# Kernel optimization log

Measured on AMD Instinct MI355X. Metric: run time of the kernel, lower is better.

## Reference

```python
import jax, jax.numpy as jnp
import numpy as np

N = 50000      # n_nodes
S = 16         # neighbors per node
D_IN = 256     # raw feature dim
PREP = 128     # prep_len
H = 2          # n_head
OUT = 64       # per-head spec output_dim (concat_node doubles it)
MP = 2         # n_mp (metapaths)
IN2 = 2 * OUT * H  # layer-2 input dim = 256


def setup_inputs() -> dict:
    key = jax.random.key(0)
    ks = jax.random.split(key, 7)
    feats = jax.random.normal(ks[0], (N, D_IN), jnp.float32)
    prep_W = jax.random.normal(ks[1], (D_IN, PREP), jnp.float32) * 0.05
    Wx1 = jax.random.normal(ks[2], (MP, H, PREP, OUT), jnp.float32) * 0.05
    Wn1 = jax.random.normal(ks[3], (MP, H, PREP, OUT), jnp.float32) * 0.05
    Wx2 = jax.random.normal(ks[4], (MP, H, IN2, OUT), jnp.float32) * 0.05
    Wn2 = jax.random.normal(ks[5], (MP, H, IN2, OUT), jnp.float32) * 0.05
    node_neigh = jax.random.randint(ks[6], (MP, N, S), 0, N, dtype=jnp.int32)
    return {"feats": feats, "prep_W": prep_W, "Wx1": Wx1, "Wn1": Wn1,
            "Wx2": Wx2, "Wn2": Wn2, "node_neigh": node_neigh}


def _agg_layer(x, neigh, Wx, Wn):
    # x: [N, d]; neigh: [N, S]; Wx, Wn: [H, d, OUT]
    # neighbor gather + mean (the chunk_edge = all_feats[node_neigh] path)
    agg = jnp.mean(x[neigh], axis=1)                  # [N, d]
    xh = jnp.einsum('nd,hdo->nho', x, Wx)             # [N, H, OUT]
    nh = jnp.einsum('nd,hdo->nho', agg, Wn)           # [N, H, OUT]
    h = jax.nn.relu(jnp.concatenate([xh, nh], -1))    # per-head concat_node
    return h.reshape(x.shape[0], -1)                  # heads concatenated


def reference(feats, prep_W, Wx1, Wn1, Wx2, Wn2, node_neigh):
    # feats[all_ids].detach() in the original -> stop_gradient
    feats = jax.lax.stop_gradient(feats)
    outs = []
    for mp in range(MP):
        h0 = feats @ prep_W                           # prep (dummy == layer-1 prep here)
        neigh = node_neigh[mp]
        h1 = _agg_layer(h0, neigh, Wx1[mp], Wn1[mp])  # [N, 256]
        h2 = _agg_layer(h1, neigh, Wx2[mp], Wn2[mp])  # [N, 256]
        outs.append(jnp.concatenate([h1, h2], axis=-1))  # skip-buffer concat
    return jnp.stack(outs, axis=0)                    # [MP, N, 512]
```

## Files before the change

### kernel.cpp

```cpp
#include <hip/hip_runtime.h>

#define NN 50000
#define SNEI 16
#define GB 782

typedef unsigned short ushort_t;
typedef unsigned int uint_t;
typedef unsigned long long u64;
typedef __attribute__((ext_vector_type(8))) short bhalf8;
typedef __attribute__((ext_vector_type(4))) float facc4;
typedef __attribute__((ext_vector_type(4))) float f32x4;
typedef __attribute__((ext_vector_type(4))) int i32x4;
typedef __attribute__((ext_vector_type(4))) uint_t u32x4;

__device__ __forceinline__ float b2f(uint_t u) {
    union { uint_t u; float f; } x; x.u = u << 16; return x.f;
}
__device__ __forceinline__ ushort_t f2b(float f) {
    union { float f; uint_t u; } x; x.f = f;
    return (ushort_t)((x.u + 0x7FFFu + ((x.u >> 16) & 1u)) >> 16);
}
__device__ __forceinline__ u64 pack4(float a, float b, float c, float d) {
    return (u64)f2b(a) | ((u64)f2b(b) << 16) | ((u64)f2b(c) << 32) | ((u64)f2b(d) << 48);
}

typedef const __attribute__((address_space(1))) void cglb_t;
typedef __attribute__((address_space(3))) void lds3_t;
__device__ __forceinline__ void gload16(const void* g, void* l) {
    __builtin_amdgcn_global_load_lds((cglb_t*)g, (lds3_t*)l, 16, 0, 0);
}

__global__ void permSetup(const float* __restrict__ prepW,
                          const float* __restrict__ Wx1, const float* __restrict__ Wn1,
                          const float* __restrict__ Wx2, const float* __restrict__ Wn2,
                          ushort_t* __restrict__ dst)
{
    int e = blockIdx.x * 256 + threadIdx.x;
    int q8 = e >> 3, j = e & 7;
    int layer = q8 >> 14;
    int qq = q8 & 16383;
    int mp = qq >> 13, isN = (qq >> 12) & 1, q = qq & 4095;
    int lane = q & 63, nf = (q >> 6) & 7, ks = q >> 9;
    int c = nf * 16 + (lane & 15);
    int k = ks * 32 + ((lane >> 4) << 3) + j;
    float v;
    if (layer == 0) {
        const float* W1 = (isN ? Wn1 : Wx1) + mp * 16384 + (c >> 6) * 8192 + (c & 63);
        const float* pw = prepW + (size_t)k * 128;
        float s0 = 0.f, s1 = 0.f;
#pragma unroll 4
        for (int p = 0; p < 128; p += 2) {
            s0 += pw[p]     * W1[(size_t)p * 64];
            s1 += pw[p + 1] * W1[(size_t)(p + 1) * 64];
        }
        v = s0 + s1;
    } else {
        const float* W2 = (isN ? Wn2 : Wx2) + mp * 32768 + (c >> 6) * 16384 + (size_t)k * 64 + (c & 63);
        v = *W2;
    }
    dst[(size_t)q8 * 8 + j] = f2b(v);
}

__global__ __launch_bounds__(512, 4)
void proj1_gemm(const float* __restrict__ X,
                const ushort_t* __restrict__ W, size_t wMpStr,
                float* __restrict__ out, size_t oMpStr,
                ushort_t* __restrict__ h1, size_t hMpStr,
                ushort_t* __restrict__ P, size_t PMpStr)
{
    __shared__ bhalf8 lds[4608];
    u64* l64 = (u64*)lds;
    const int tid = threadIdx.x;
    const int lane = tid & 63;
    const int wid = tid >> 6;
    const int wave_m = wid >> 2;
    const int role = wid & 3;
    const int mp = role >> 1, isN = role & 1;
    const int m0 = blockIdx.x * 64;

    facc4 acc[2][8];
    const facc4 z = {0.f, 0.f, 0.f, 0.f};
#pragma unroll
    for (int i = 0; i < 2; ++i)
#pragma unroll
        for (int j = 0; j < 8; ++j) acc[i][j] = z;

    for (int kt = 0; kt < 4; ++kt) {
        {
            int s = tid;
            int fp = s >> 6, ls = s & 63;
            int mf = fp & 3, ksl = fp >> 2;
            int row = m0 + mf * 16 + (ls & 15); if (row > NN - 1) row = NN - 1;
            const f32x4* gp = (const f32x4*)(X + (size_t)row * 256 + kt * 64 + ksl * 32 + ((ls >> 4) << 3));
            f32x4 f0 = gp[0], f1 = gp[1];
            l64[s * 2]     = pack4(f0[0], f0[1], f0[2], f0[3]);
            l64[s * 2 + 1] = pack4(f1[0], f1[1], f1[2], f1[3]);
        }
#pragma unroll
        for (int it = 0; it < 8; ++it) {
            int c4 = it * 512 + tid;
            int m = c4 >> 10, c = c4 & 1023;
            const ushort_t* src = W + (size_t)(m >> 1) * wMpStr + (m & 1) * 32768
                                + ((size_t)kt * 1024 + c) * 8;
            gload16(src, (char*)lds + (512 + m * 1024 + c) * 16);
        }
        __syncthreads();
        const int wB = 512 + role * 1024;
#pragma unroll
        for (int ksl = 0; ksl < 2; ++ksl) {
            bhalf8 a0 = lds[(ksl * 4 + wave_m * 2 + 0) * 64 + lane];
            bhalf8 a1 = lds[(ksl * 4 + wave_m * 2 + 1) * 64 + lane];
#pragma unroll
            for (int nf = 0; nf < 8; ++nf) {
                bhalf8 b = lds[wB + (ksl * 8 + nf) * 64 + lane];
                acc[0][nf] = __builtin_amdgcn_mfma_f32_16x16x32_bf16(a0, b, acc[0][nf], 0, 0, 0);
                acc[1][nf] = __builtin_amdgcn_mfma_f32_16x16x32_bf16(a1, b, acc[1][nf], 0, 0, 0);
            }
        }
        __syncthreads();
    }
    const int cl = lane & 15, rg = lane >> 4;
    if (isN == 0) {
        float* xl = (float*)lds + mp * (64 * 132);
#pragma unroll
        for (int mf2 = 0; mf2 < 2; ++mf2) {
            int rowl = (wave_m * 2 + mf2) * 16 + rg * 4;
#pragma unroll
            for (int nf = 0; nf < 8; ++nf) {
                int cpr = nf * 16 + cl;
                facc4 v = acc[mf2][nf];
#pragma unroll
                for (int rr = 0; rr < 4; ++rr)
                    xl[(rowl + rr) * 132 + cpr] = fmaxf(v[rr], 0.0f);
            }
        }
    } else {
        ushort_t* Pp = P + (size_t)mp * PMpStr;
#pragma unroll
        for (int mf2 = 0; mf2 < 2; ++mf2) {
            int rowb = m0 + (wave_m * 2 + mf2) * 16 + rg * 4;
#pragma unroll
            for (int nf = 0; nf < 8; ++nf) {
                int cpr = nf * 16 + cl;
                facc4 v = acc[mf2][nf];
#pragma unroll
                for (int rr = 0; rr < 4; ++rr) {
                    int row = rowb + rr;
                    if (row < NN)
                        Pp[(size_t)(cpr >> 5) * (NN * 32) + (size_t)row * 32 + (cpr & 31)] = f2b(v[rr]);
                }
            }
        }
    }
    __syncthreads();
#pragma unroll
    for (int it = 0; it < 8; ++it) {
        int u = it * 512 + tid;
        int seg = u >> 4, l16 = u & 15;
        int mp2 = seg >> 7, rowl = (seg >> 1) & 63, ch = seg & 1;
        int row = m0 + rowl;
        f32x4 v = *(f32x4*)((float*)lds + mp2 * (64 * 132) + rowl * 132 + ch * 64 + l16 * 4);
        if (row < NN) {
            __builtin_nontemporal_store(v,
                (f32x4*)(out + (size_t)mp2 * oMpStr + (size_t)row * 512 + ch * 128 + l16 * 4));
            *(u64*)(h1 + (size_t)mp2 * hMpStr + (size_t)row * 256 + ch * 128 + l16 * 4)
                = pack4(v[0], v[1], v[2], v[3]);
        }
    }
}

__global__ __launch_bounds__(256, 4)
void proj2_gemm(const ushort_t* __restrict__ X, size_t xMpStr,
                const ushort_t* __restrict__ W, size_t wMpStr,
                float* __restrict__ out, size_t oMpStr,
                ushort_t* __restrict__ P, size_t PMpStr)
{
    __shared__ bhalf8 lds[2560];
    const int tid = threadIdx.x;
    const int lane = tid & 63;
    const int wid = tid >> 6;
    const int wave_m = wid >> 1, wave_n = wid & 1;
    const int m0 = blockIdx.x * 64;
    const int mp = blockIdx.y;

    const ushort_t* Xp = X + (size_t)mp * xMpStr;
    const ushort_t* wx = W + (size_t)mp * wMpStr;
    const ushort_t* wn = wx + 4096 * 8;
    float* outp = out + (size_t)mp * oMpStr;
    ushort_t* Pp = P + (size_t)mp * PMpStr;

    facc4 acc[2][8];
    const facc4 z = {0.f, 0.f, 0.f, 0.f};
#pragma unroll
    for (int i = 0; i < 2; ++i)
#pragma unroll
        for (int j = 0; j < 8; ++j) acc[i][j] = z;

    for (int kt = 0; kt < 4; ++kt) {
#pragma unroll
        for (int it = 0; it < 2; ++it) {
            int u = wid + it * 4;
            int mf = u & 3, ksl = u >> 2;
            int row = m0 + mf * 16 + (lane & 15); if (row > NN - 1) row = NN - 1;
            const ushort_t* src = Xp + (size_t)row * 256 + kt * 64 + ksl * 32 + ((lane >> 4) << 3);
            gload16(src, (char*)lds + (u * 64 + lane) * 16);
        }
#pragma unroll
        for (int it = 0; it < 4; ++it) {
            int cb = (it * 4 + wid) * 64;
            gload16(wx + ((size_t)kt * 1024 + cb + lane) * 8,
                    (char*)lds + (512 + cb + lane) * 16);
            gload16(wn + ((size_t)kt * 1024 + cb + lane) * 8,
                    (char*)lds + (1536 + cb + lane) * 16);
        }
        __syncthreads();
        const int wB = wave_n ? 1536 : 512;
#pragma unroll
        for (int ksl = 0; ksl < 2; ++ksl) {
            bhalf8 a0 = lds[(ksl * 4 + wave_m * 2 + 0) * 64 + lane];
            bhalf8 a1 = lds[(ksl * 4 + wave_m * 2 + 1) * 64 + lane];
#pragma unroll
            for (int nf = 0; nf < 8; ++nf) {
                bhalf8 b = lds[wB + (ksl * 8 + nf) * 64 + lane];
                acc[0][nf] = __builtin_amdgcn_mfma_f32_16x16x32_bf16(a0, b, acc[0][nf], 0, 0, 0);
                acc[1][nf] = __builtin_amdgcn_mfma_f32_16x16x32_bf16(a1, b, acc[1][nf], 0, 0, 0);
            }
        }
        __syncthreads();
    }
    const int cl = lane & 15, rg = lane >> 4;
    float* xl = (float*)lds;
    if (wave_n == 0) {
#pragma unroll
        for (int mf2 = 0; mf2 < 2; ++mf2) {
            int rowl = (wave_m * 2 + mf2) * 16 + rg * 4;
#pragma unroll
            for (int nf = 0; nf < 8; ++nf) {
                int cpr = nf * 16 + cl;
                facc4 v = acc[mf2][nf];
#pragma unroll
                for (int rr = 0; rr < 4; ++rr)
                    xl[(rowl + rr) * 132 + cpr] = fmaxf(v[rr], 0.0f);
            }
        }
    } else {
#pragma unroll
        for (int mf2 = 0; mf2 < 2; ++mf2) {
            int rowb = m0 + (wave_m * 2 + mf2) * 16 + rg * 4;
#pragma unroll
            for (int nf = 0; nf < 8; ++nf) {
                int cpr = nf * 16 + cl;
                facc4 v = acc[mf2][nf];
#pragma unroll
                for (int rr = 0; rr < 4; ++rr) {
                    int row = rowb + rr;
                    if (row < NN)
                        Pp[(size_t)(cpr >> 5) * (NN * 32) + (size_t)row * 32 + (cpr & 31)] = f2b(v[rr]);
                }
            }
        }
    }
    __syncthreads();
#pragma unroll
    for (int j = 0; j < 4; ++j) {
        int rowl2 = wid * 16 + j * 4 + (lane >> 4);
        int row = m0 + rowl2;
#pragma unroll
        for (int c = 0; c < 2; ++c) {
            f32x4 v = *(f32x4*)&xl[rowl2 * 132 + c * 64 + cl * 4];
            if (row < NN)
                __builtin_nontemporal_store(v,
                    (f32x4*)&outp[(size_t)row * 512 + 256 + c * 128 + cl * 4]);
        }
    }
}

template<bool WRH1>
__global__ __launch_bounds__(256)
void gatherS(const ushort_t* __restrict__ P, size_t PMpStr,
             const int* __restrict__ nb, size_t nMpStr,
             float* __restrict__ out, size_t oMpStr, int obase,
             ushort_t* __restrict__ h1, size_t hMpStr)
{
    const int b = blockIdx.x;
    const int pair = b & 7;
    const int slice = pair & 3, mp = pair >> 2;
    const int nodeBase = (b >> 3) * 64;

    const ushort_t* Pp = P + (size_t)mp * PMpStr + (size_t)slice * (NN * 32);
    const int* nbp = nb + (size_t)mp * nMpStr;
    float* outp = out + (size_t)mp * oMpStr;

    __shared__ int nls[1024];
    __shared__ float og[64 * 36];
    {
        int i4 = nodeBase * 4 + threadIdx.x;
        int mx = NN * 4 - 1;
        if (i4 > mx) i4 = mx;
        i32x4 v = __builtin_nontemporal_load((const i32x4*)nbp + i4);
        ((i32x4*)nls)[threadIdx.x] = v;
    }
    __syncthreads();

    const int nl = threadIdx.x >> 2, q = threadIdx.x & 3;
    const int node = nodeBase + nl;
    const int* nr = nls + nl * SNEI;
    float a0=0.f,a1=0.f,a2=0.f,a3=0.f,a4=0.f,a5=0.f,a6=0.f,a7=0.f;
#pragma unroll
    for (int s = 0; s < SNEI; ++s) {
        u32x4 v = *(const u32x4*)(Pp + (size_t)nr[s] * 32 + q * 8);
        a0 += b2f(v.x & 0xFFFFu); a1 += b2f(v.x >> 16);
        a2 += b2f(v.y & 0xFFFFu); a3 += b2f(v.y >> 16);
        a4 += b2f(v.z & 0xFFFFu); a5 += b2f(v.z >> 16);
        a6 += b2f(v.w & 0xFFFFu); a7 += b2f(v.w >> 16);
    }
    const float M = 0.0625f;
    f32x4 r0 = { fmaxf(a0*M, 0.f), fmaxf(a1*M, 0.f), fmaxf(a2*M, 0.f), fmaxf(a3*M, 0.f) };
    f32x4 r1 = { fmaxf(a4*M, 0.f), fmaxf(a5*M, 0.f), fmaxf(a6*M, 0.f), fmaxf(a7*M, 0.f) };
    const int cco = (slice >> 1) * 128 + 64 + (slice & 1) * 32 + q * 8;
    if constexpr (WRH1) {
        if (node < NN) {
            ushort_t* hp = h1 + (size_t)mp * hMpStr + (size_t)node * 256 + cco;
            *(u64*)hp       = pack4(r0[0], r0[1], r0[2], r0[3]);
            *(u64*)(hp + 4) = pack4(r1[0], r1[1], r1[2], r1[3]);
        }
    }
    *(f32x4*)&og[nl * 36 + q * 8]     = r0;
    *(f32x4*)&og[nl * 36 + q * 8 + 4] = r1;
    __syncthreads();

    const int coff0 = (slice >> 1) * 128 + 64 + (slice & 1) * 32;
#pragma unroll
    for (int it = 0; it < 2; ++it) {
        int rl = it * 32 + (threadIdx.x >> 3), sub = threadIdx.x & 7;
        int nd = nodeBase + rl;
        f32x4 v = *(f32x4*)&og[rl * 36 + sub * 4];
        if (nd < NN)
            __builtin_nontemporal_store(v,
                (f32x4*)(outp + (size_t)nd * 512 + obase + coff0 + sub * 4));
    }
}

extern "C" void kernel_launch(void* const* d_in, const int* in_sizes, int n_in,
                              void* d_out, int out_size, void* d_ws, size_t ws_size,
                              hipStream_t stream)
{
    const float* feats  = (const float*)d_in[0];
    const float* prepWp = (const float*)d_in[1];
    const float* Wx1    = (const float*)d_in[2];
    const float* Wn1    = (const float*)d_in[3];
    const float* Wx2    = (const float*)d_in[4];
    const float* Wn2    = (const float*)d_in[5];
    const int*   neigh  = (const int*)d_in[6];
    float* out = (float*)d_out;
    ushort_t* ws = (ushort_t*)d_ws;

    const size_t permElems = 262144;
    ushort_t* perm = ws;
    ushort_t* P    = ws + permElems;
    ushort_t* h1   = P + 2 * (size_t)NN * 128;

    const size_t PStr = (size_t)NN * 128;
    const size_t hStr = (size_t)NN * 256;
    const size_t oStr = (size_t)NN * 512;
    const size_t nStr = (size_t)NN * SNEI;
    const size_t wStr = (size_t)8192 * 8;

    permSetup<<<1024, 256, 0, stream>>>(prepWp, Wx1, Wn1, Wx2, Wn2, perm);

    proj1_gemm<<<GB, 512, 0, stream>>>(feats, perm, wStr,
                                       out, oStr, h1, hStr, P, PStr);
    gatherS<true><<<GB * 8, 256, 0, stream>>>(P, PStr, neigh, nStr,
                                              out, oStr, 0, h1, hStr);
    proj2_gemm<<<dim3(GB, 2), 256, 0, stream>>>(h1, hStr,
                                                perm + (size_t)16384 * 8, wStr,
                                                out, oStr, P, PStr);
    gatherS<false><<<GB * 8, 256, 0, stream>>>(P, PStr, neigh, nStr,
                                               out, oStr, 256, nullptr, 0);
}
```

Before: 173.7 us.

## Fuse layer-1 neighbor gather into layer-2 projection kernel

```diff
diff --git a/kernel.cpp b/kernel.cpp
--- a/kernel.cpp
+++ b/kernel.cpp
@@ -65,8 +65,8 @@
 void proj1_gemm(const float* __restrict__ X,
                 const ushort_t* __restrict__ W, size_t wMpStr,
                 float* __restrict__ out, size_t oMpStr,
-                ushort_t* __restrict__ h1, size_t hMpStr,
-                ushort_t* __restrict__ P, size_t PMpStr)
+                ushort_t* __restrict__ h1x, size_t hMpStr,
+                ushort_t* __restrict__ P1, size_t PMpStr)
 {
     __shared__ bhalf8 lds[4608];
     u64* l64 = (u64*)lds;
@@ -135,7 +135,7 @@
             }
         }
     } else {
-        ushort_t* Pp = P + (size_t)mp * PMpStr;
+        ushort_t* Pp = P1 + (size_t)mp * PMpStr;
 #pragma unroll
         for (int mf2 = 0; mf2 < 2; ++mf2) {
             int rowb = m0 + (wave_m * 2 + mf2) * 16 + rg * 4;
@@ -147,7 +147,7 @@
                 for (int rr = 0; rr < 4; ++rr) {
                     int row = rowb + rr;
                     if (row < NN)
-                        Pp[(size_t)(cpr >> 5) * (NN * 32) + (size_t)row * 32 + (cpr & 31)] = f2b(v[rr]);
+                        Pp[(size_t)row * 128 + cpr] = f2b(v[rr]);
                 }
             }
         }
@@ -163,17 +163,19 @@
         if (row < NN) {
             __builtin_nontemporal_store(v,
                 (f32x4*)(out + (size_t)mp2 * oMpStr + (size_t)row * 512 + ch * 128 + l16 * 4));
-            *(u64*)(h1 + (size_t)mp2 * hMpStr + (size_t)row * 256 + ch * 128 + l16 * 4)
+            *(u64*)(h1x + (size_t)mp2 * hMpStr + (size_t)row * 128 + ch * 64 + l16 * 4)
                 = pack4(v[0], v[1], v[2], v[3]);
         }
     }
 }
 
 __global__ __launch_bounds__(256, 4)
-void proj2_gemm(const ushort_t* __restrict__ X, size_t xMpStr,
-                const ushort_t* __restrict__ W, size_t wMpStr,
-                float* __restrict__ out, size_t oMpStr,
-                ushort_t* __restrict__ P, size_t PMpStr)
+void proj2f(const ushort_t* __restrict__ h1x, size_t hMpStr,
+            const ushort_t* __restrict__ P1, size_t P1MpStr,
+            const int* __restrict__ nb, size_t nMpStr,
+            const ushort_t* __restrict__ W, size_t wMpStr,
+            float* __restrict__ out, size_t oMpStr,
+            ushort_t* __restrict__ P2, size_t P2MpStr)
 {
     __shared__ bhalf8 lds[2560];
     const int tid = threadIdx.x;
@@ -183,11 +185,57 @@
     const int m0 = blockIdx.x * 64;
     const int mp = blockIdx.y;
 
-    const ushort_t* Xp = X + (size_t)mp * xMpStr;
+    const ushort_t* hx = h1x + (size_t)mp * hMpStr;
+    const ushort_t* Pp1 = P1 + (size_t)mp * P1MpStr;
+    const int* nbp = nb + (size_t)mp * nMpStr;
     const ushort_t* wx = W + (size_t)mp * wMpStr;
     const ushort_t* wn = wx + 4096 * 8;
     float* outp = out + (size_t)mp * oMpStr;
-    ushort_t* Pp = P + (size_t)mp * PMpStr;
+    ushort_t* Pp2 = P2 + (size_t)mp * P2MpStr;
+
+    int* nls = (int*)lds;
+    {
+        int i4 = m0 * 4 + tid;
+        int mx = NN * 4 - 1;
+        if (i4 > mx) i4 = mx;
+        ((i32x4*)nls)[tid] = __builtin_nontemporal_load((const i32x4*)nbp + i4);
+    }
+    __syncthreads();
+
+    const int nl = tid >> 2, q = tid & 3;
+    const int node = m0 + nl;
+    const int* nr = nls + nl * SNEI;
+    float ac[32];
+#pragma unroll
+    for (int i = 0; i < 32; ++i) ac[i] = 0.f;
+#pragma unroll 4
+    for (int s = 0; s < SNEI; ++s) {
+        const ushort_t* src = Pp1 + (size_t)nr[s] * 128 + q * 32;
+#pragma unroll
+        for (int g = 0; g < 4; ++g) {
+            u32x4 v = *(const u32x4*)(src + g * 8);
+            ac[g*8+0] += b2f(v.x & 0xFFFFu); ac[g*8+1] += b2f(v.x >> 16);
+            ac[g*8+2] += b2f(v.y & 0xFFFFu); ac[g*8+3] += b2f(v.y >> 16);
+            ac[g*8+4] += b2f(v.z & 0xFFFFu); ac[g*8+5] += b2f(v.z >> 16);
+            ac[g*8+6] += b2f(v.w & 0xFFFFu); ac[g*8+7] += b2f(v.w >> 16);
+        }
+    }
+    const float M = 0.0625f;
+#pragma unroll
+    for (int i = 0; i < 32; ++i) ac[i] = fmaxf(ac[i] * M, 0.f);
+    if (node < NN) {
+        float* o = outp + (size_t)node * 512 + (q >> 1) * 128 + 64 + (q & 1) * 32;
+#pragma unroll
+        for (int g = 0; g < 8; ++g) {
+            f32x4 v = { ac[g*4], ac[g*4+1], ac[g*4+2], ac[g*4+3] };
+            __builtin_nontemporal_store(v, (f32x4*)(o + g * 4));
+        }
+    }
+    u64 st[8];
+#pragma unroll
+    for (int g = 0; g < 8; ++g)
+        st[g] = pack4(ac[g*4], ac[g*4+1], ac[g*4+2], ac[g*4+3]);
+    __syncthreads();
 
     facc4 acc[2][8];
     const facc4 z = {0.f, 0.f, 0.f, 0.f};
@@ -197,13 +245,25 @@
         for (int j = 0; j < 8; ++j) acc[i][j] = z;
 
     for (int kt = 0; kt < 4; ++kt) {
-#pragma unroll
-        for (int it = 0; it < 2; ++it) {
-            int u = wid + it * 4;
-            int mf = u & 3, ksl = u >> 2;
-            int row = m0 + mf * 16 + (lane & 15); if (row > NN - 1) row = NN - 1;
-            const ushort_t* src = Xp + (size_t)row * 256 + kt * 64 + ksl * 32 + ((lane >> 4) << 3);
-            gload16(src, (char*)lds + (u * 64 + lane) * 16);
+        if ((kt & 1) == 0) {
+#pragma unroll
+            for (int it = 0; it < 2; ++it) {
+                int u = wid + it * 4;
+                int mf = u & 3, ksl = u >> 2;
+                int row = m0 + mf * 16 + (lane & 15); if (row > NN - 1) row = NN - 1;
+                const ushort_t* src = hx + (size_t)row * 128 + (kt >> 1) * 64 + ksl * 32 + ((lane >> 4) << 3);
+                gload16(src, (char*)lds + (u * 64 + lane) * 16);
+            }
+        } else {
+            if ((q >> 1) == (kt >> 1)) {
+                int ksl = q & 1, r = nl;
+#pragma unroll
+                for (int g = 0; g < 4; ++g) {
+                    int chunk = (ksl * 4 + (r >> 4)) * 64 + g * 16 + (r & 15);
+                    u64* d = (u64*)&lds[chunk];
+                    d[0] = st[g * 2]; d[1] = st[g * 2 + 1];
+                }
+            }
         }
 #pragma unroll
         for (int it = 0; it < 4; ++it) {
@@ -255,7 +315,7 @@
                 for (int rr = 0; rr < 4; ++rr) {
                     int row = rowb + rr;
                     if (row < NN)
-                        Pp[(size_t)(cpr >> 5) * (NN * 32) + (size_t)row * 32 + (cpr & 31)] = f2b(v[rr]);
+                        Pp2[(size_t)(cpr >> 5) * (NN * 32) + (size_t)row * 32 + (cpr & 31)] = f2b(v[rr]);
                 }
             }
         }
@@ -275,12 +335,10 @@
     }
 }
 
-template<bool WRH1>
 __global__ __launch_bounds__(256)
 void gatherS(const ushort_t* __restrict__ P, size_t PMpStr,
              const int* __restrict__ nb, size_t nMpStr,
-             float* __restrict__ out, size_t oMpStr, int obase,
-             ushort_t* __restrict__ h1, size_t hMpStr)
+             float* __restrict__ out, size_t oMpStr)
 {
     const int b = blockIdx.x;
     const int pair = b & 7;
@@ -297,13 +355,11 @@
         int i4 = nodeBase * 4 + threadIdx.x;
         int mx = NN * 4 - 1;
         if (i4 > mx) i4 = mx;
-        i32x4 v = __builtin_nontemporal_load((const i32x4*)nbp + i4);
-        ((i32x4*)nls)[threadIdx.x] = v;
+        ((i32x4*)nls)[threadIdx.x] = __builtin_nontemporal_load((const i32x4*)nbp + i4);
     }
     __syncthreads();
 
     const int nl = threadIdx.x >> 2, q = threadIdx.x & 3;
-    const int node = nodeBase + nl;
     const int* nr = nls + nl * SNEI;
     float a0=0.f,a1=0.f,a2=0.f,a3=0.f,a4=0.f,a5=0.f,a6=0.f,a7=0.f;
 #pragma unroll
@@ -317,14 +373,6 @@
     const float M = 0.0625f;
     f32x4 r0 = { fmaxf(a0*M, 0.f), fmaxf(a1*M, 0.f), fmaxf(a2*M, 0.f), fmaxf(a3*M, 0.f) };
     f32x4 r1 = { fmaxf(a4*M, 0.f), fmaxf(a5*M, 0.f), fmaxf(a6*M, 0.f), fmaxf(a7*M, 0.f) };
-    const int cco = (slice >> 1) * 128 + 64 + (slice & 1) * 32 + q * 8;
-    if constexpr (WRH1) {
-        if (node < NN) {
-            ushort_t* hp = h1 + (size_t)mp * hMpStr + (size_t)node * 256 + cco;
-            *(u64*)hp       = pack4(r0[0], r0[1], r0[2], r0[3]);
-            *(u64*)(hp + 4) = pack4(r1[0], r1[1], r1[2], r1[3]);
-        }
-    }
     *(f32x4*)&og[nl * 36 + q * 8]     = r0;
     *(f32x4*)&og[nl * 36 + q * 8 + 4] = r1;
     __syncthreads();
@@ -337,7 +385,7 @@
         f32x4 v = *(f32x4*)&og[rl * 36 + sub * 4];
         if (nd < NN)
             __builtin_nontemporal_store(v,
-                (f32x4*)(outp + (size_t)nd * 512 + obase + coff0 + sub * 4));
+                (f32x4*)(outp + (size_t)nd * 512 + 256 + coff0 + sub * 4));
     }
 }
 
@@ -356,12 +404,12 @@
     ushort_t* ws = (ushort_t*)d_ws;
 
     const size_t permElems = 262144;
+    const size_t NP = (size_t)NN * 128;
     ushort_t* perm = ws;
-    ushort_t* P    = ws + permElems;
-    ushort_t* h1   = P + 2 * (size_t)NN * 128;
-
-    const size_t PStr = (size_t)NN * 128;
-    const size_t hStr = (size_t)NN * 256;
+    ushort_t* P1   = ws + permElems;
+    ushort_t* P2   = P1 + 2 * NP;
+    ushort_t* h1x  = P2 + 2 * NP;
+
     const size_t oStr = (size_t)NN * 512;
     const size_t nStr = (size_t)NN * SNEI;
     const size_t wStr = (size_t)8192 * 8;
@@ -369,12 +417,9 @@
     permSetup<<<1024, 256, 0, stream>>>(prepWp, Wx1, Wn1, Wx2, Wn2, perm);
 
     proj1_gemm<<<GB, 512, 0, stream>>>(feats, perm, wStr,
-                                       out, oStr, h1, hStr, P, PStr);
-    gatherS<true><<<GB * 8, 256, 0, stream>>>(P, PStr, neigh, nStr,
-                                              out, oStr, 0, h1, hStr);
-    proj2_gemm<<<dim3(GB, 2), 256, 0, stream>>>(h1, hStr,
-                                                perm + (size_t)16384 * 8, wStr,
-                                                out, oStr, P, PStr);
-    gatherS<false><<<GB * 8, 256, 0, stream>>>(P, PStr, neigh, nStr,
-                                               out, oStr, 256, nullptr, 0);
-}
+                                       out, oStr, h1x, NP, P1, NP);
+    proj2f<<<dim3(GB, 2), 256, 0, stream>>>(h1x, NP, P1, NP, neigh, nStr,
+                                            perm + (size_t)16384 * 8, wStr,
+                                            out, oStr, P2, NP);
+    gatherS<<<GB * 8, 256, 0, stream>>>(P2, NP, neigh, nStr, out, oStr);
+}
```

Result: slower. 223.0 us (+28.4%).
